# Optimization experiments

Measured on AMD Instinct MI355X. Metric: run time of the kernel, lower is better.

## Reference

```python
import jax, jax.numpy as jnp
import numpy as np

B, C, N, Hdim, Wdim = 32, 64, 16384, 128, 128  # N = Hdim*Wdim, C = dim = num_embeddings
EPS = 1e-5


def setup_inputs() -> dict:
    key = jax.random.key(0)
    ks = jax.random.split(key, 6)
    s = 0.05  # weight scale
    return {
        "x": jax.random.normal(ks[0], (B, C, N), dtype=jnp.float32),
        "Wq": jax.random.normal(ks[1], (C, C), dtype=jnp.float32) * s,   # Conv1d q (1x1)
        "bq": jnp.zeros((C,), jnp.float32),
        "gamma": jnp.ones((C,), jnp.float32),                              # BatchNorm1d affine
        "beta": jnp.zeros((C,), jnp.float32),
        "Wq2": jax.random.normal(ks[2], (C, C), dtype=jnp.float32) * s,  # Conv1d q2 (1x1)
        "bq2": jnp.zeros((C,), jnp.float32),
        "Wsr": jax.random.normal(ks[3], (C, C), dtype=jnp.float32) * s,  # Conv2d sr, k=1,s=1 -> 1x1
        "bsr": jnp.zeros((C,), jnp.float32),
        "Wc": jax.random.normal(ks[4], (C, C), dtype=jnp.float32) * s,   # Conv1d conv (1x1, no bias)
        "H": Hdim,
        "W": Wdim,
    }


def reference(x, Wq, bq, gamma, beta, Wq2, bq2, Wsr, bsr, Wc, H, W):
    # x: (B, C, N), N = H*W, sr_ratio = 1
    # q = q2(BN(q(x))) -- all 1x1 convs; BN uses batch statistics (torch training mode)
    q = jnp.einsum('oc,bcn->bon', Wq, x) + bq[None, :, None]            # (B,C,N)
    mu = q.mean(axis=(0, 2), keepdims=True)
    var = q.var(axis=(0, 2), keepdims=True)
    q = (q - mu) * jax.lax.rsqrt(var + EPS)
    q = q * gamma[None, :, None] + beta[None, :, None]
    q = jnp.einsum('oc,bcn->bon', Wq2, q) + bq2[None, :, None]          # (B,C,N)

    # k = sr(x) with kernel/stride 1 -> 1x1 conv, then permute to (B,N,C)
    k = jnp.einsum('oc,bcn->bon', Wsr, x) + bsr[None, :, None]          # (B,C,N)

    # v = AvgPool1d(C) over the channel axis of x^T -> channel mean, (B,1,N)
    v = x.mean(axis=1, keepdims=True)                                    # (B,1,N)

    # attn = q @ k^T over the N axis -> (B,C,C), then MaxPool1d(C) -> row-wise max (B,C,1)
    attn = jnp.einsum('bcn,bdn->bcd', q, k)                              # (B,C,C)
    attn = attn.max(axis=-1, keepdims=True)                              # (B,C,1)

    # out = conv( attn @ v )  -- outer product broadcast, then 1x1 conv (no bias)
    out = attn * v                                                       # (B,C,N)
    out = jnp.einsum('oc,bcn->bon', Wc, out)                             # (B,C,N)
    return out
```

## Files before the change

kernel.cpp:

```cpp
#include <hip/hip_runtime.h>
#include <hip/hip_bf16.h>

#define B_ 32
#define C_ 64
#define N_ 16384
constexpr float BN_INV = 1.0f / (32.0f * 16384.0f);

typedef float f32x4 __attribute__((ext_vector_type(4)));
typedef short s16x8 __attribute__((ext_vector_type(8)));

constexpr size_t WS_GPART = 0;
constexpr size_t WS_RPART = WS_GPART + (size_t)512 * 4096;
constexpr size_t WS_G     = WS_RPART + (size_t)512 * 64;
constexpr size_t WS_RB    = WS_G + (size_t)32 * 4096;
constexpr size_t WS_V     = WS_RB + (size_t)32 * 64;
constexpr size_t WS_W     = WS_V + (size_t)32 * N_;
constexpr size_t WS_GBAR  = WS_W + (size_t)32 * 64;
constexpr size_t WS_MBAR  = WS_GBAR + 4096;

__device__ constexpr int P1I[10] = {0,0,0,0,1,1,1,2,2,3};
__device__ constexpr int P1J[10] = {0,1,2,3,1,2,3,2,3,3};
__device__ constexpr int P1AT[4][4] = {{0,1,2,3},{1,4,5,6},{2,5,7,8},{3,6,8,9}};

__device__ __forceinline__ unsigned short bf16_rne_s(float f) {
    unsigned u = __float_as_uint(f);
    unsigned r = u + 0x7FFFu + ((u >> 16) & 1u);
    return (unsigned short)(r >> 16);
}
__device__ __forceinline__ float bf16f(unsigned short u) {
    return __uint_as_float(((unsigned)u) << 16);
}
__device__ __forceinline__ unsigned cvt_pk_bf16(float lo, float hi) {
    unsigned r;
    asm("v_cvt_pk_bf16_f32 %0, %1, %2" : "=v"(r) : "v"(lo), "v"(hi));
    return r;
}
__device__ __forceinline__ void cvt8hi(const f32x4& a, const f32x4& b, s16x8& hi) {
    union { unsigned w[4]; s16x8 v; } u;
    u.w[0] = cvt_pk_bf16(a[0], a[1]);
    u.w[1] = cvt_pk_bf16(a[2], a[3]);
    u.w[2] = cvt_pk_bf16(b[0], b[1]);
    u.w[3] = cvt_pk_bf16(b[2], b[3]);
    hi = u.v;
}

__global__ __launch_bounds__(512, 2) void k1(const float* __restrict__ x, float* __restrict__ ws) {
    __shared__ __align__(16) float rawb[4][10 * 256];
    __shared__ float rws[8][64];
    const int t = threadIdx.x, wv = t >> 6, lane = t & 63;
    const int b = blockIdx.x >> 4, ch = blockIdx.x & 15;
    const int kg = lane >> 4, cl = lane & 15;
    const float* xb = x + ((size_t)b * C_ + cl) * N_ + ch * 1024 + kg * 8;

    if (blockIdx.x == 0) {
        #pragma unroll
        for (int i = 0; i < 8; ++i) ws[WS_GBAR + t * 8 + i] = 0.f;
        if (t < 64) ws[WS_MBAR + t] = 0.f;
    }

    f32x4 accP1[10];
    #pragma unroll
    for (int i = 0; i < 10; ++i) accP1[i] = (f32x4){0.f, 0.f, 0.f, 0.f};
    f32x4 rs = {0.f, 0.f, 0.f, 0.f};

    f32x4 cA[4], cB[4], nA[4], nB[4];
    #pragma unroll
    for (int g = 0; g < 4; ++g) {
        cA[g] = *(const f32x4*)(xb + (size_t)g * (16 * N_) + wv * 32);
        cB[g] = *(const f32x4*)(xb + (size_t)g * (16 * N_) + wv * 32 + 4);
    }

    for (int w = 0; w < 4; ++w) {
        if (w < 3) {
            const int noff = (8 * (w + 1) + wv) * 32;
            #pragma unroll
            for (int g = 0; g < 4; ++g) {
                nA[g] = *(const f32x4*)(xb + (size_t)g * (16 * N_) + noff);
                nB[g] = *(const f32x4*)(xb + (size_t)g * (16 * N_) + noff + 4);
            }
        }
        s16x8 hi[4];
        #pragma unroll
        for (int g = 0; g < 4; ++g) cvt8hi(cA[g], cB[g], hi[g]);

        f32x4 s0 = cA[0] + cA[1] + cA[2] + cA[3];
        f32x4 s1 = cB[0] + cB[1] + cB[2] + cB[3];
        #pragma unroll
        for (int m = 1; m <= 8; m <<= 1) {
            #pragma unroll
            for (int j = 0; j < 4; ++j) {
                s0[j] += __shfl_xor(s0[j], m);
                s1[j] += __shfl_xor(s1[j], m);
            }
        }
        if (cl == 0) {
            float* vp = ws + WS_V + (size_t)b * N_ + ch * 1024 + (8 * w + wv) * 32 + kg * 8;
            *(f32x4*)vp       = s0 * 0.015625f;
            *(f32x4*)(vp + 4) = s1 * 0.015625f;
        }
        #pragma unroll
        for (int g = 0; g < 4; ++g)
            rs[g] += cA[g][0] + cA[g][1] + cA[g][2] + cA[g][3]
                   + cB[g][0] + cB[g][1] + cB[g][2] + cB[g][3];

        #pragma unroll
        for (int i = 0; i < 10; ++i)
            accP1[i] = __builtin_amdgcn_mfma_f32_16x16x32_bf16(hi[P1I[i]], hi[P1J[i]], accP1[i], 0, 0, 0);

        #pragma unroll
        for (int g = 0; g < 4; ++g) { cA[g] = nA[g]; cB[g] = nB[g]; }
    }

    #pragma unroll
    for (int g = 0; g < 4; ++g) {
        rs[g] += __shfl_xor(rs[g], 16);
        rs[g] += __shfl_xor(rs[g], 32);
    }
    if (lane < 16) {
        #pragma unroll
        for (int g = 0; g < 4; ++g) rws[wv][g * 16 + lane] = rs[g];
    }

    if (wv < 4) {
        float* dst = rawb[wv];
        #pragma unroll
        for (int i = 0; i < 10; ++i) *(f32x4*)(dst + i * 256 + lane * 4) = accP1[i];
    }
    __syncthreads();
    if (wv >= 4) {
        float* dst = rawb[wv - 4];
        #pragma unroll
        for (int i = 0; i < 10; ++i) {
            f32x4 o = *(f32x4*)(dst + i * 256 + lane * 4);
            *(f32x4*)(dst + i * 256 + lane * 4) = o + accP1[i];
        }
    }
    __syncthreads();
    if (t < 64) {
        float s = 0.f;
        #pragma unroll
        for (int g = 0; g < 8; ++g) s += rws[g][t];
        ws[WS_RPART + (size_t)blockIdx.x * 64 + t] = s;
    }
    float* gp = ws + WS_GPART + (size_t)blockIdx.x * 4096;
    for (int e = t; e < 4096; e += 512) {
        const int r = e >> 6, c = e & 63;
        const int bi = r >> 4, bj = c >> 4, rr = r & 15, cc = c & 15;
        const int i1 = P1AT[bi][bj] * 256;
        const int o1 = (bi <= bj) ? (((rr >> 2) * 16 + cc) * 4 + (rr & 3))
                                  : (((cc >> 2) * 16 + rr) * 4 + (cc & 3));
        gp[e] = rawb[0][i1 + o1] + rawb[1][i1 + o1] + rawb[2][i1 + o1] + rawb[3][i1 + o1];
    }
}

__global__ __launch_bounds__(256) void k2a(float* __restrict__ ws) {
    const int b = blockIdx.x >> 3, sl = blockIdx.x & 7, t = threadIdx.x;
    #pragma unroll
    for (int h = 0; h < 2; ++h) {
        const int e = sl * 512 + h * 256 + t;
        float s = 0.f;
        for (int chn = 0; chn < 16; ++chn) s += ws[WS_GPART + ((size_t)(b * 16 + chn)) * 4096 + e];
        ws[WS_G + (size_t)b * 4096 + e] = s;
        unsafeAtomicAdd(ws + WS_GBAR + e, s);
    }
    if (sl == 0 && t < 64) {
        float s = 0.f;
        for (int chn = 0; chn < 16; ++chn) s += ws[WS_RPART + (size_t)(b * 16 + chn) * 64 + t];
        ws[WS_RB + b * 64 + t] = s;
        unsafeAtomicAdd(ws + WS_MBAR + t, s);
    }
}

__global__ __launch_bounds__(256) void k2b(const float* __restrict__ Wq, const float* __restrict__ gamma,
                                           const float* __restrict__ beta, const float* __restrict__ Wq2,
                                           const float* __restrict__ bq2, const float* __restrict__ Wsr,
                                           const float* __restrict__ bsr, const float* __restrict__ Wc,
                                           float* __restrict__ ws) {
    __shared__ __align__(16) unsigned short OPH[6][64 * 72];
    __shared__ float quadS[64], muS[64], DS[64], abv[64], mS[64];
    __shared__ float rl[64], ul[64], avs[64], sbv[64], pls[64], aml[64];
    const int bb = blockIdx.x, t = threadIdx.x;
    const int w = t >> 6, lane = t & 63, cl = lane & 15, jg = lane >> 4;
    const int sr = t >> 2, sc0 = (t & 3) * 16;

    {
        const float* srcs[5] = { ws + WS_GBAR, Wq, Wq2, ws + WS_G + (size_t)bb * 4096, Wsr };
        #pragma unroll
        for (int mI = 0; mI < 5; ++mI) {
            const float sc = (mI == 0) ? BN_INV : 1.f;
            const float* src = srcs[mI] + sr * 64 + sc0;
            s16x8 h8[2];
            #pragma unroll
            for (int q = 0; q < 2; ++q) {
                f32x4 a = *(const f32x4*)(src + q * 8);
                f32x4 b2 = *(const f32x4*)(src + q * 8 + 4);
                #pragma unroll
                for (int j = 0; j < 8; ++j)
                    h8[q][j] = (short)bf16_rne_s(((j < 4) ? a[j] : b2[j - 4]) * sc);
            }
            *(s16x8*)(&OPH[mI][sr * 72 + sc0])     = h8[0];
            *(s16x8*)(&OPH[mI][sr * 72 + sc0 + 8]) = h8[1];
        }
    }
    if (t < 64) {
        mS[t]  = ws[WS_MBAR + t] * BN_INV;
        rl[t]  = ws[WS_RB + bb * 64 + t];
        sbv[t] = bsr[t];
    }
    __syncthreads();

    auto mmStripe = [&](const unsigned short* AH, const unsigned short* BH, int row0, f32x4* acc) {
        #pragma unroll
        for (int ks = 0; ks < 2; ++ks) {
            const int ko = ks * 32 + jg * 8;
            s16x8 ah = *(const s16x8*)(AH + (row0 + cl) * 72 + ko);
            #pragma unroll
            for (int bj = 0; bj < 4; ++bj) {
                s16x8 bh = *(const s16x8*)(BH + (16 * bj + cl) * 72 + ko);
                acc[bj] = __builtin_amdgcn_mfma_f32_16x16x32_bf16(ah, bh, acc[bj], 0, 0, 0);
            }
        }
    };

    if (w < 2) {
        f32x4 acc2[2][4];
        #pragma unroll
        for (int st = 0; st < 2; ++st)
            #pragma unroll
            for (int i = 0; i < 4; ++i) acc2[st][i] = (f32x4){0.f, 0.f, 0.f, 0.f};
        mmStripe(OPH[1], OPH[0], 32 * w,      acc2[0]);
        mmStripe(OPH[1], OPH[0], 32 * w + 16, acc2[1]);
        #pragma unroll
        for (int st = 0; st < 2; ++st) {
            float s[4] = {0.f, 0.f, 0.f, 0.f};
            #pragma unroll
            for (int j = 0; j < 4; ++j) {
                const int row = 32 * w + 16 * st + jg * 4 + j;
                #pragma unroll
                for (int bj = 0; bj < 4; ++bj)
                    s[j] += acc2[st][bj][j] * bf16f(OPH[1][row * 72 + 16 * bj + cl]);
            }
            #pragma unroll
            for (int m = 1; m <= 8; m <<= 1)
                #pragma unroll
                for (int j = 0; j < 4; ++j) s[j] += __shfl_xor(s[j], m);
            if (cl == 0) {
                #pragma unroll
                for (int j = 0; j < 4; ++j) quadS[32 * w + 16 * st + jg * 4 + j] = s[j];
            }
        }
        if (t < 64) {
            float s2 = 0.f;
            #pragma unroll 8
            for (int c = 0; c < 64; ++c) s2 += bf16f(OPH[1][t * 72 + c]) * mS[c];
            muS[t] = s2;
        }
    } else {
        const int w2 = w - 2;
        f32x4 acc2[2][4];
        #pragma unroll
        for (int st = 0; st < 2; ++st)
            #pragma unroll
            for (int i = 0; i < 4; ++i) acc2[st][i] = (f32x4){0.f, 0.f, 0.f, 0.f};
        mmStripe(OPH[4], OPH[3], 32 * w2,      acc2[0]);
        mmStripe(OPH[4], OPH[3], 32 * w2 + 16, acc2[1]);
        #pragma unroll
        for (int st = 0; st < 2; ++st)
            #pragma unroll
            for (int bj = 0; bj < 4; ++bj)
                #pragma unroll
                for (int j = 0; j < 4; ++j) {
                    const int row = 32 * w2 + 16 * st + jg * 4 + j, col = 16 * bj + cl;
                    OPH[5][row * 72 + col] = (unsigned short)bf16_rne_s(acc2[st][bj][j]);
                }
        const int t2 = t - 128;
        if (t2 < 64) {
            float s = 0.f;
            #pragma unroll 8
            for (int k = 0; k < 64; ++k) s += bf16f(OPH[4][t2 * 72 + k]) * rl[k];
            pls[t2] = s + 16384.f * sbv[t2];
        }
    }
    __syncthreads();

    if (t < 64) {
        const float var = quadS[t] - muS[t] * muS[t];
        const float D = gamma[t] * rsqrtf(var + 1e-5f);
        DS[t] = D;
        abv[t] = beta[t] - D * muS[t];
    }
    __syncthreads();
    {
        #pragma unroll
        for (int q = 0; q < 2; ++q) {
            s16x8 h8;
            #pragma unroll
            for (int j = 0; j < 8; ++j) {
                const int c = sc0 + q * 8 + j;
                h8[j] = (short)bf16_rne_s(DS[c] * bf16f(OPH[1][c * 72 + sr]));
            }
            *(s16x8*)(&OPH[0][sr * 72 + sc0 + q * 8]) = h8;
        }
    }
    if (t < 64) {
        float s = 0.f;
        #pragma unroll 8
        for (int k = 0; k < 64; ++k) s += bf16f(OPH[2][t * 72 + k]) * abv[k];
        avs[t] = s + bq2[t];
    }
    __syncthreads();

    {
        f32x4 accA[4];
        #pragma unroll
        for (int i = 0; i < 4; ++i) accA[i] = (f32x4){0.f, 0.f, 0.f, 0.f};
        mmStripe(OPH[2], OPH[0], 16 * w, accA);
        float su[4] = {0.f, 0.f, 0.f, 0.f};
        #pragma unroll
        for (int bj = 0; bj < 4; ++bj) {
            const float cv = rl[16 * bj + cl];
            #pragma unroll
            for (int j = 0; j < 4; ++j) su[j] += accA[bj][j] * cv;
        }
        #pragma unroll
        for (int m = 1; m <= 8; m <<= 1)
            #pragma unroll
            for (int j = 0; j < 4; ++j) su[j] += __shfl_xor(su[j], m);
        if (cl == 0) {
            #pragma unroll
            for (int j = 0; j < 4; ++j) ul[16 * w + jg * 4 + j] = su[j];
        }
        #pragma unroll
        for (int bj = 0; bj < 4; ++bj)
            #pragma unroll
            for (int j = 0; j < 4; ++j) {
                const int row = 16 * w + jg * 4 + j, col = 16 * bj + cl;
                OPH[1][row * 72 + col] = (unsigned short)bf16_rne_s(accA[bj][j]);
            }
    }
    __syncthreads();

    {
        f32x4 acc[4];
        #pragma unroll
        for (int i = 0; i < 4; ++i) acc[i] = (f32x4){0.f, 0.f, 0.f, 0.f};
        mmStripe(OPH[1], OPH[5], 16 * w, acc);
        float mx[4] = {-3.4e38f, -3.4e38f, -3.4e38f, -3.4e38f};
        #pragma unroll
        for (int j = 0; j < 4; ++j) {
            const int row = 16 * w + jg * 4 + j;
            const float ur = ul[row], ar = avs[row];
            #pragma unroll
            for (int bj = 0; bj < 4; ++bj) {
                const int col = 16 * bj + cl;
                const float v = acc[bj][j] + ur * sbv[col] + ar * pls[col];
                mx[j] = fmaxf(mx[j], v);
            }
        }
        #pragma unroll
        for (int m = 1; m <= 8; m <<= 1)
            #pragma unroll
            for (int j = 0; j < 4; ++j) mx[j] = fmaxf(mx[j], __shfl_xor(mx[j], m));
        if (cl == 0) {
            #pragma unroll
            for (int j = 0; j < 4; ++j) aml[16 * w + jg * 4 + j] = mx[j];
        }
    }
    __syncthreads();

    if (t < 64) {
        float s = 0.f;
        #pragma unroll 8
        for (int c = 0; c < 64; ++c) s += Wc[t * 64 + c] * aml[c];
        ws[WS_W + bb * 64 + t] = s;
    }
}

__global__ __launch_bounds__(256) void k3(const float* __restrict__ ws, float* __restrict__ out) {
    const int blk = blockIdx.x;
    const int b = blk >> 6, seg = blk & 63;
    const int r0 = (seg >> 4) * 16, chk = seg & 15;
    __shared__ float wls[16];
    const int t = threadIdx.x;
    if (t < 16) wls[t] = ws[WS_W + b * 64 + r0 + t];
    __syncthreads();
    const size_t nb = (size_t)chk * 1024 + 4 * t;
    const f32x4 v4 = *(const f32x4*)(ws + WS_V + (size_t)b * N_ + nb);
    float* ob = out + ((size_t)b * C_ + r0) * N_ + nb;
    #pragma unroll
    for (int o = 0; o < 16; ++o) {
        __builtin_nontemporal_store(v4 * wls[o], (f32x4*)(ob + (size_t)o * N_));
    }
}

extern "C" void kernel_launch(void* const* d_in, const int* in_sizes, int n_in,
                              void* d_out, int out_size, void* d_ws, size_t ws_size,
                              hipStream_t stream) {
    const float* x     = (const float*)d_in[0];
    const float* Wq    = (const float*)d_in[1];
    const float* gamma = (const float*)d_in[3];
    const float* beta  = (const float*)d_in[4];
    const float* Wq2   = (const float*)d_in[5];
    const float* bq2   = (const float*)d_in[6];
    const float* Wsr   = (const float*)d_in[7];
    const float* bsr   = (const float*)d_in[8];
    const float* Wc    = (const float*)d_in[9];
    float* ws  = (float*)d_ws;
    float* out = (float*)d_out;

    hipLaunchKernelGGL(k1,  dim3(512),  dim3(512), 0, stream, x, ws);
    hipLaunchKernelGGL(k2a, dim3(256),  dim3(256), 0, stream, ws);
    hipLaunchKernelGGL(k2b, dim3(32),   dim3(256), 0, stream,
                       Wq, gamma, beta, Wq2, bq2, Wsr, bsr, Wc, ws);
    hipLaunchKernelGGL(k3,  dim3(2048), dim3(256), 0, stream, ws, out);
}
```

Baseline: 68.91 us.

## Fuse reduction, chain and broadcast kernels into one cooperative kernel with grid syncs

```diff
diff --git a/kernel.cpp b/kernel.cpp
--- a/kernel.cpp
+++ b/kernel.cpp
@@ -1,5 +1,8 @@
 #include <hip/hip_runtime.h>
 #include <hip/hip_bf16.h>
+#include <hip/hip_cooperative_groups.h>
+
+namespace cg = cooperative_groups;
 
 #define B_ 32
 #define C_ 64
@@ -153,35 +156,38 @@
     }
 }
 
-__global__ __launch_bounds__(256) void k2a(float* __restrict__ ws) {
-    const int b = blockIdx.x >> 3, sl = blockIdx.x & 7, t = threadIdx.x;
-    #pragma unroll
-    for (int h = 0; h < 2; ++h) {
-        const int e = sl * 512 + h * 256 + t;
-        float s = 0.f;
-        for (int chn = 0; chn < 16; ++chn) s += ws[WS_GPART + ((size_t)(b * 16 + chn)) * 4096 + e];
-        ws[WS_G + (size_t)b * 4096 + e] = s;
-        unsafeAtomicAdd(ws + WS_GBAR + e, s);
-    }
+
+__device__ __forceinline__ void phaseA_body(int blk, int t, float* __restrict__ ws) {
+    const int b = blk >> 4, sl = blk & 15;
+    const int e = sl * 256 + t;
+    float s = 0.f;
+    #pragma unroll 4
+    for (int chn = 0; chn < 16; ++chn) s += ws[WS_GPART + ((size_t)(b * 16 + chn)) * 4096 + e];
+    ws[WS_G + (size_t)b * 4096 + e] = s;
+    unsafeAtomicAdd(ws + WS_GBAR + e, s);
     if (sl == 0 && t < 64) {
-        float s = 0.f;
-        for (int chn = 0; chn < 16; ++chn) s += ws[WS_RPART + (size_t)(b * 16 + chn) * 64 + t];
-        ws[WS_RB + b * 64 + t] = s;
-        unsafeAtomicAdd(ws + WS_MBAR + t, s);
-    }
-}
-
-__global__ __launch_bounds__(256) void k2b(const float* __restrict__ Wq, const float* __restrict__ gamma,
+        float s2 = 0.f;
+        #pragma unroll 4
+        for (int chn = 0; chn < 16; ++chn) s2 += ws[WS_RPART + (size_t)(b * 16 + chn) * 64 + t];
+        ws[WS_RB + b * 64 + t] = s2;
+        unsafeAtomicAdd(ws + WS_MBAR + t, s2);
+    }
+}
+
+__device__ __forceinline__ void chain_body(int bb, int t, unsigned short* __restrict__ OPH,
+                                           float* __restrict__ SV,
+                                           const float* __restrict__ Wq, const float* __restrict__ gamma,
                                            const float* __restrict__ beta, const float* __restrict__ Wq2,
                                            const float* __restrict__ bq2, const float* __restrict__ Wsr,
                                            const float* __restrict__ bsr, const float* __restrict__ Wc,
                                            float* __restrict__ ws) {
-    __shared__ __align__(16) unsigned short OPH[6][64 * 72];
-    __shared__ float quadS[64], muS[64], DS[64], abv[64], mS[64];
-    __shared__ float rl[64], ul[64], avs[64], sbv[64], pls[64], aml[64];
-    const int bb = blockIdx.x, t = threadIdx.x;
+    float* quadS = SV;        float* muS = SV + 64;  float* DS  = SV + 128;
+    float* abv   = SV + 192;  float* mS  = SV + 256; float* rl  = SV + 320;
+    float* ul    = SV + 384;  float* avs = SV + 448; float* sbv = SV + 512;
+    float* pls   = SV + 576;  float* aml = SV + 640;
     const int w = t >> 6, lane = t & 63, cl = lane & 15, jg = lane >> 4;
     const int sr = t >> 2, sc0 = (t & 3) * 16;
+    auto SLOT = [&](int i) { return OPH + i * 4608; };
 
     {
         const float* srcs[5] = { ws + WS_GBAR, Wq, Wq2, ws + WS_G + (size_t)bb * 4096, Wsr };
@@ -198,8 +204,8 @@
                 for (int j = 0; j < 8; ++j)
                     h8[q][j] = (short)bf16_rne_s(((j < 4) ? a[j] : b2[j - 4]) * sc);
             }
-            *(s16x8*)(&OPH[mI][sr * 72 + sc0])     = h8[0];
-            *(s16x8*)(&OPH[mI][sr * 72 + sc0 + 8]) = h8[1];
+            *(s16x8*)(SLOT(mI) + sr * 72 + sc0)     = h8[0];
+            *(s16x8*)(SLOT(mI) + sr * 72 + sc0 + 8) = h8[1];
         }
     }
     if (t < 64) {
@@ -228,8 +234,8 @@
         for (int st = 0; st < 2; ++st)
             #pragma unroll
             for (int i = 0; i < 4; ++i) acc2[st][i] = (f32x4){0.f, 0.f, 0.f, 0.f};
-        mmStripe(OPH[1], OPH[0], 32 * w,      acc2[0]);
-        mmStripe(OPH[1], OPH[0], 32 * w + 16, acc2[1]);
+        mmStripe(SLOT(1), SLOT(0), 32 * w,      acc2[0]);
+        mmStripe(SLOT(1), SLOT(0), 32 * w + 16, acc2[1]);
         #pragma unroll
         for (int st = 0; st < 2; ++st) {
             float s[4] = {0.f, 0.f, 0.f, 0.f};
@@ -238,7 +244,7 @@
                 const int row = 32 * w + 16 * st + jg * 4 + j;
                 #pragma unroll
                 for (int bj = 0; bj < 4; ++bj)
-                    s[j] += acc2[st][bj][j] * bf16f(OPH[1][row * 72 + 16 * bj + cl]);
+                    s[j] += acc2[st][bj][j] * bf16f(SLOT(1)[row * 72 + 16 * bj + cl]);
             }
             #pragma unroll
             for (int m = 1; m <= 8; m <<= 1)
@@ -252,7 +258,7 @@
         if (t < 64) {
             float s2 = 0.f;
             #pragma unroll 8
-            for (int c = 0; c < 64; ++c) s2 += bf16f(OPH[1][t * 72 + c]) * mS[c];
+            for (int c = 0; c < 64; ++c) s2 += bf16f(SLOT(1)[t * 72 + c]) * mS[c];
             muS[t] = s2;
         }
     } else {
@@ -262,8 +268,8 @@
         for (int st = 0; st < 2; ++st)
             #pragma unroll
             for (int i = 0; i < 4; ++i) acc2[st][i] = (f32x4){0.f, 0.f, 0.f, 0.f};
-        mmStripe(OPH[4], OPH[3], 32 * w2,      acc2[0]);
-        mmStripe(OPH[4], OPH[3], 32 * w2 + 16, acc2[1]);
+        mmStripe(SLOT(4), SLOT(3), 32 * w2,      acc2[0]);
+        mmStripe(SLOT(4), SLOT(3), 32 * w2 + 16, acc2[1]);
         #pragma unroll
         for (int st = 0; st < 2; ++st)
             #pragma unroll
@@ -271,13 +277,13 @@
                 #pragma unroll
                 for (int j = 0; j < 4; ++j) {
                     const int row = 32 * w2 + 16 * st + jg * 4 + j, col = 16 * bj + cl;
-                    OPH[5][row * 72 + col] = (unsigned short)bf16_rne_s(acc2[st][bj][j]);
+                    SLOT(5)[row * 72 + col] = (unsigned short)bf16_rne_s(acc2[st][bj][j]);
                 }
         const int t2 = t - 128;
-        if (t2 < 64) {
+        if (t2 < 64 && t2 >= 0) {
             float s = 0.f;
             #pragma unroll 8
-            for (int k = 0; k < 64; ++k) s += bf16f(OPH[4][t2 * 72 + k]) * rl[k];
+            for (int k = 0; k < 64; ++k) s += bf16f(SLOT(4)[t2 * 72 + k]) * rl[k];
             pls[t2] = s + 16384.f * sbv[t2];
         }
     }
@@ -297,15 +303,15 @@
             #pragma unroll
             for (int j = 0; j < 8; ++j) {
                 const int c = sc0 + q * 8 + j;
-                h8[j] = (short)bf16_rne_s(DS[c] * bf16f(OPH[1][c * 72 + sr]));
-            }
-            *(s16x8*)(&OPH[0][sr * 72 + sc0 + q * 8]) = h8;
+                h8[j] = (short)bf16_rne_s(DS[c] * bf16f(SLOT(1)[c * 72 + sr]));
+            }
+            *(s16x8*)(SLOT(0) + sr * 72 + sc0 + q * 8) = h8;
         }
     }
     if (t < 64) {
         float s = 0.f;
         #pragma unroll 8
-        for (int k = 0; k < 64; ++k) s += bf16f(OPH[2][t * 72 + k]) * abv[k];
+        for (int k = 0; k < 64; ++k) s += bf16f(SLOT(2)[t * 72 + k]) * abv[k];
         avs[t] = s + bq2[t];
     }
     __syncthreads();
@@ -314,7 +320,7 @@
         f32x4 accA[4];
         #pragma unroll
         for (int i = 0; i < 4; ++i) accA[i] = (f32x4){0.f, 0.f, 0.f, 0.f};
-        mmStripe(OPH[2], OPH[0], 16 * w, accA);
+        mmStripe(SLOT(2), SLOT(0), 16 * w, accA);
         float su[4] = {0.f, 0.f, 0.f, 0.f};
         #pragma unroll
         for (int bj = 0; bj < 4; ++bj) {
@@ -335,7 +341,7 @@
             #pragma unroll
             for (int j = 0; j < 4; ++j) {
                 const int row = 16 * w + jg * 4 + j, col = 16 * bj + cl;
-                OPH[1][row * 72 + col] = (unsigned short)bf16_rne_s(accA[bj][j]);
+                SLOT(1)[row * 72 + col] = (unsigned short)bf16_rne_s(accA[bj][j]);
             }
     }
     __syncthreads();
@@ -344,7 +350,7 @@
         f32x4 acc[4];
         #pragma unroll
         for (int i = 0; i < 4; ++i) acc[i] = (f32x4){0.f, 0.f, 0.f, 0.f};
-        mmStripe(OPH[1], OPH[5], 16 * w, acc);
+        mmStripe(SLOT(1), SLOT(5), 16 * w, acc);
         float mx[4] = {-3.4e38f, -3.4e38f, -3.4e38f, -3.4e38f};
         #pragma unroll
         for (int j = 0; j < 4; ++j) {
@@ -376,21 +382,58 @@
     }
 }
 
-__global__ __launch_bounds__(256) void k3(const float* __restrict__ ws, float* __restrict__ out) {
-    const int blk = blockIdx.x;
-    const int b = blk >> 6, seg = blk & 63;
-    const int r0 = (seg >> 4) * 16, chk = seg & 15;
-    __shared__ float wls[16];
-    const int t = threadIdx.x;
-    if (t < 16) wls[t] = ws[WS_W + b * 64 + r0 + t];
+__device__ __forceinline__ void phaseC_body(int blk, int t, float* __restrict__ wls,
+                                            const float* __restrict__ ws, float* __restrict__ out) {
+    const int b = blk >> 4, chk = blk & 15;
+    if (t < 64) wls[t] = ws[WS_W + b * 64 + t];
     __syncthreads();
     const size_t nb = (size_t)chk * 1024 + 4 * t;
     const f32x4 v4 = *(const f32x4*)(ws + WS_V + (size_t)b * N_ + nb);
-    float* ob = out + ((size_t)b * C_ + r0) * N_ + nb;
+    float* ob = out + (size_t)b * C_ * N_ + nb;
     #pragma unroll
-    for (int o = 0; o < 16; ++o) {
+    for (int o = 0; o < 64; ++o) {
         __builtin_nontemporal_store(v4 * wls[o], (f32x4*)(ob + (size_t)o * N_));
     }
+}
+
+__global__ __launch_bounds__(256, 2) void k2x(const float* __restrict__ Wq, const float* __restrict__ gamma,
+                                              const float* __restrict__ beta, const float* __restrict__ Wq2,
+                                              const float* __restrict__ bq2, const float* __restrict__ Wsr,
+                                              const float* __restrict__ bsr, const float* __restrict__ Wc,
+                                              float* __restrict__ ws, float* __restrict__ out) {
+    __shared__ __align__(16) unsigned char smem[58112];
+    cg::grid_group grid = cg::this_grid();
+    const int t = threadIdx.x;
+
+    phaseA_body(blockIdx.x, t, ws);
+    __threadfence();
+    grid.sync();
+
+    if (blockIdx.x < 32) {
+        chain_body(blockIdx.x, t, (unsigned short*)smem, (float*)(smem + 55296),
+                   Wq, gamma, beta, Wq2, bq2, Wsr, bsr, Wc, ws);
+    }
+    __threadfence();
+    grid.sync();
+
+    phaseC_body(blockIdx.x, t, (float*)smem, ws, out);
+}
+
+__global__ __launch_bounds__(256) void k2a(float* __restrict__ ws) {
+    phaseA_body(blockIdx.x, threadIdx.x, ws);
+}
+__global__ __launch_bounds__(256) void k2b(const float* __restrict__ Wq, const float* __restrict__ gamma,
+                                           const float* __restrict__ beta, const float* __restrict__ Wq2,
+                                           const float* __restrict__ bq2, const float* __restrict__ Wsr,
+                                           const float* __restrict__ bsr, const float* __restrict__ Wc,
+                                           float* __restrict__ ws) {
+    __shared__ __align__(16) unsigned char smem[58112];
+    chain_body(blockIdx.x, threadIdx.x, (unsigned short*)smem, (float*)(smem + 55296),
+               Wq, gamma, beta, Wq2, bq2, Wsr, bsr, Wc, ws);
+}
+__global__ __launch_bounds__(256) void k3(const float* __restrict__ ws, float* __restrict__ out) {
+    __shared__ float wls[64];
+    phaseC_body(blockIdx.x, threadIdx.x, wls, ws, out);
 }
 
 extern "C" void kernel_launch(void* const* d_in, const int* in_sizes, int n_in,
@@ -408,9 +451,16 @@
     float* ws  = (float*)d_ws;
     float* out = (float*)d_out;
 
-    hipLaunchKernelGGL(k1,  dim3(512),  dim3(512), 0, stream, x, ws);
-    hipLaunchKernelGGL(k2a, dim3(256),  dim3(256), 0, stream, ws);
-    hipLaunchKernelGGL(k2b, dim3(32),   dim3(256), 0, stream,
-                       Wq, gamma, beta, Wq2, bq2, Wsr, bsr, Wc, ws);
-    hipLaunchKernelGGL(k3,  dim3(2048), dim3(256), 0, stream, ws, out);
-}
+    hipLaunchKernelGGL(k1, dim3(512), dim3(512), 0, stream, x, ws);
+
+    void* args[] = {(void*)&Wq, (void*)&gamma, (void*)&beta, (void*)&Wq2, (void*)&bq2,
+                    (void*)&Wsr, (void*)&bsr, (void*)&Wc, (void*)&ws, (void*)&out};
+    hipError_t err = hipLaunchCooperativeKernel((void*)k2x, dim3(512), dim3(256), args, 0, stream);
+    if (err != hipSuccess) {
+        (void)hipGetLastError();
+        hipLaunchKernelGGL(k2a, dim3(512), dim3(256), 0, stream, ws);
+        hipLaunchKernelGGL(k2b, dim3(32),  dim3(256), 0, stream,
+                           Wq, gamma, beta, Wq2, bq2, Wsr, bsr, Wc, ws);
+        hipLaunchKernelGGL(k3,  dim3(512), dim3(256), 0, stream, ws, out);
+    }
+}
```

Measured after the change: 238.0 us. 245% more time.

## Fuse Gram reduction and per-batch solve into one cooperative kernel

Applied to the files above, without the earlier changes.

```diff
diff --git a/kernel.cpp b/kernel.cpp
--- a/kernel.cpp
+++ b/kernel.cpp
@@ -1,5 +1,8 @@
 #include <hip/hip_runtime.h>
 #include <hip/hip_bf16.h>
+#include <hip/hip_cooperative_groups.h>
+
+namespace cg = cooperative_groups;
 
 #define B_ 32
 #define C_ 64
@@ -17,6 +20,8 @@
 constexpr size_t WS_W     = WS_V + (size_t)32 * N_;
 constexpr size_t WS_GBAR  = WS_W + (size_t)32 * 64;
 constexpr size_t WS_MBAR  = WS_GBAR + 4096;
+constexpr size_t WS_QUAD  = WS_MBAR + 64;
+constexpr size_t WS_MACC  = WS_QUAD + 64;
 
 __device__ constexpr int P1I[10] = {0,0,0,0,1,1,1,2,2,3};
 __device__ constexpr int P1J[10] = {0,1,2,3,1,2,3,2,3,3};
@@ -55,7 +60,11 @@
     if (blockIdx.x == 0) {
         #pragma unroll
         for (int i = 0; i < 8; ++i) ws[WS_GBAR + t * 8 + i] = 0.f;
-        if (t < 64) ws[WS_MBAR + t] = 0.f;
+        if (t < 64) {
+            ws[WS_MBAR + t] = 0.f;
+            ws[WS_QUAD + t] = 0.f;
+            ws[WS_MACC + t] = 0.f;
+        }
     }
 
     f32x4 accP1[10];
@@ -150,6 +159,238 @@
         const int o1 = (bi <= bj) ? (((rr >> 2) * 16 + cc) * 4 + (rr & 3))
                                   : (((cc >> 2) * 16 + rr) * 4 + (cc & 3));
         gp[e] = rawb[0][i1 + o1] + rawb[1][i1 + o1] + rawb[2][i1 + o1] + rawb[3][i1 + o1];
+    }
+}
+
+__global__ __launch_bounds__(256, 2) void k2bc(const float* __restrict__ Wq, const float* __restrict__ gamma,
+                                               const float* __restrict__ beta, const float* __restrict__ Wq2,
+                                               const float* __restrict__ bq2, const float* __restrict__ Wsr,
+                                               const float* __restrict__ bsr, const float* __restrict__ Wc,
+                                               float* __restrict__ ws) {
+    __shared__ __align__(16) unsigned short OPH[6][64 * 72];
+    __shared__ float quadS[64], muS[64], DS[64], abv[64], mS[64];
+    __shared__ float rl[64], ul[64], avs[64], sbv[64], pls[64], aml[64];
+    cg::grid_group grid = cg::this_grid();
+    const int bb = blockIdx.x, t = threadIdx.x;
+    const int w = t >> 6, lane = t & 63, cl = lane & 15, jg = lane >> 4;
+    const int sr = t >> 2, sc0 = (t & 3) * 16;
+
+    {
+        f32x4 s[4];
+        #pragma unroll
+        for (int j = 0; j < 4; ++j) s[j] = (f32x4){0.f, 0.f, 0.f, 0.f};
+        for (int chn = 0; chn < 16; ++chn) {
+            const float* gbp = ws + WS_GPART + ((size_t)(bb * 16 + chn)) * 4096 + sr * 64 + sc0;
+            #pragma unroll
+            for (int j = 0; j < 4; ++j) s[j] += *(const f32x4*)(gbp + 4 * j);
+        }
+        s16x8 h8[2];
+        #pragma unroll
+        for (int q = 0; q < 2; ++q)
+            #pragma unroll
+            for (int j = 0; j < 8; ++j)
+                h8[q][j] = (short)bf16_rne_s(s[q * 2 + (j >> 2)][j & 3]);
+        *(s16x8*)(&OPH[3][sr * 72 + sc0])     = h8[0];
+        *(s16x8*)(&OPH[3][sr * 72 + sc0 + 8]) = h8[1];
+    }
+    {
+        const float* srcs[3] = { Wq, Wq2, Wsr };
+        const int slot[3] = {1, 2, 4};
+        #pragma unroll
+        for (int mI = 0; mI < 3; ++mI) {
+            const float* src = srcs[mI] + sr * 64 + sc0;
+            s16x8 h8[2];
+            #pragma unroll
+            for (int q = 0; q < 2; ++q) {
+                f32x4 a = *(const f32x4*)(src + q * 8);
+                f32x4 b2 = *(const f32x4*)(src + q * 8 + 4);
+                #pragma unroll
+                for (int j = 0; j < 8; ++j)
+                    h8[q][j] = (short)bf16_rne_s((j < 4) ? a[j] : b2[j - 4]);
+            }
+            *(s16x8*)(&OPH[slot[mI]][sr * 72 + sc0])     = h8[0];
+            *(s16x8*)(&OPH[slot[mI]][sr * 72 + sc0 + 8]) = h8[1];
+        }
+    }
+    if (t < 64) {
+        float s = 0.f;
+        #pragma unroll 4
+        for (int chn = 0; chn < 16; ++chn) s += ws[WS_RPART + (size_t)(bb * 16 + chn) * 64 + t];
+        rl[t]  = s;
+        sbv[t] = bsr[t];
+        unsafeAtomicAdd(ws + WS_MACC + t, s);
+    }
+    __syncthreads();
+
+    auto mmStripe = [&](const unsigned short* AH, const unsigned short* BH, int row0, f32x4* acc) {
+        #pragma unroll
+        for (int ks = 0; ks < 2; ++ks) {
+            const int ko = ks * 32 + jg * 8;
+            s16x8 ah = *(const s16x8*)(AH + (row0 + cl) * 72 + ko);
+            #pragma unroll
+            for (int bj = 0; bj < 4; ++bj) {
+                s16x8 bh = *(const s16x8*)(BH + (16 * bj + cl) * 72 + ko);
+                acc[bj] = __builtin_amdgcn_mfma_f32_16x16x32_bf16(ah, bh, acc[bj], 0, 0, 0);
+            }
+        }
+    };
+
+    if (w < 2) {
+        f32x4 acc2[2][4];
+        #pragma unroll
+        for (int st = 0; st < 2; ++st)
+            #pragma unroll
+            for (int i = 0; i < 4; ++i) acc2[st][i] = (f32x4){0.f, 0.f, 0.f, 0.f};
+        mmStripe(OPH[1], OPH[3], 32 * w,      acc2[0]);
+        mmStripe(OPH[1], OPH[3], 32 * w + 16, acc2[1]);
+        #pragma unroll
+        for (int st = 0; st < 2; ++st) {
+            float s[4] = {0.f, 0.f, 0.f, 0.f};
+            #pragma unroll
+            for (int j = 0; j < 4; ++j) {
+                const int row = 32 * w + 16 * st + jg * 4 + j;
+                #pragma unroll
+                for (int bj = 0; bj < 4; ++bj)
+                    s[j] += acc2[st][bj][j] * bf16f(OPH[1][row * 72 + 16 * bj + cl]);
+            }
+            #pragma unroll
+            for (int m = 1; m <= 8; m <<= 1)
+                #pragma unroll
+                for (int j = 0; j < 4; ++j) s[j] += __shfl_xor(s[j], m);
+            if (cl == 0) {
+                #pragma unroll
+                for (int j = 0; j < 4; ++j)
+                    unsafeAtomicAdd(ws + WS_QUAD + 32 * w + 16 * st + jg * 4 + j, s[j]);
+            }
+        }
+    } else {
+        const int w2 = w - 2;
+        f32x4 acc2[2][4];
+        #pragma unroll
+        for (int st = 0; st < 2; ++st)
+            #pragma unroll
+            for (int i = 0; i < 4; ++i) acc2[st][i] = (f32x4){0.f, 0.f, 0.f, 0.f};
+        mmStripe(OPH[4], OPH[3], 32 * w2,      acc2[0]);
+        mmStripe(OPH[4], OPH[3], 32 * w2 + 16, acc2[1]);
+        #pragma unroll
+        for (int st = 0; st < 2; ++st)
+            #pragma unroll
+            for (int bj = 0; bj < 4; ++bj)
+                #pragma unroll
+                for (int j = 0; j < 4; ++j) {
+                    const int row = 32 * w2 + 16 * st + jg * 4 + j, col = 16 * bj + cl;
+                    OPH[5][row * 72 + col] = (unsigned short)bf16_rne_s(acc2[st][bj][j]);
+                }
+        const int t2 = t - 128;
+        if (t2 < 64 && t2 >= 0) {
+            float s = 0.f;
+            #pragma unroll 8
+            for (int k = 0; k < 64; ++k) s += bf16f(OPH[4][t2 * 72 + k]) * rl[k];
+            pls[t2] = s + 16384.f * sbv[t2];
+        }
+    }
+    __threadfence();
+    grid.sync();
+
+    if (t < 64) {
+        mS[t]    = ws[WS_MACC + t] * BN_INV;
+        quadS[t] = ws[WS_QUAD + t] * BN_INV;
+    }
+    __syncthreads();
+    if (t < 64) {
+        float s2 = 0.f;
+        #pragma unroll 8
+        for (int c = 0; c < 64; ++c) s2 += bf16f(OPH[1][t * 72 + c]) * mS[c];
+        muS[t] = s2;
+        const float var = quadS[t] - s2 * s2;
+        const float D = gamma[t] * rsqrtf(var + 1e-5f);
+        DS[t] = D;
+        abv[t] = beta[t] - D * s2;
+    }
+    __syncthreads();
+    {
+        #pragma unroll
+        for (int q = 0; q < 2; ++q) {
+            s16x8 h8;
+            #pragma unroll
+            for (int j = 0; j < 8; ++j) {
+                const int c = sc0 + q * 8 + j;
+                h8[j] = (short)bf16_rne_s(DS[c] * bf16f(OPH[1][c * 72 + sr]));
+            }
+            *(s16x8*)(&OPH[0][sr * 72 + sc0 + q * 8]) = h8;
+        }
+    }
+    if (t < 64) {
+        float s = 0.f;
+        #pragma unroll 8
+        for (int k = 0; k < 64; ++k) s += bf16f(OPH[2][t * 72 + k]) * abv[k];
+        avs[t] = s + bq2[t];
+    }
+    __syncthreads();
+
+    {
+        f32x4 accA[4];
+        #pragma unroll
+        for (int i = 0; i < 4; ++i) accA[i] = (f32x4){0.f, 0.f, 0.f, 0.f};
+        mmStripe(OPH[2], OPH[0], 16 * w, accA);
+        float su[4] = {0.f, 0.f, 0.f, 0.f};
+        #pragma unroll
+        for (int bj = 0; bj < 4; ++bj) {
+            const float cv = rl[16 * bj + cl];
+            #pragma unroll
+            for (int j = 0; j < 4; ++j) su[j] += accA[bj][j] * cv;
+        }
+        #pragma unroll
+        for (int m = 1; m <= 8; m <<= 1)
+            #pragma unroll
+            for (int j = 0; j < 4; ++j) su[j] += __shfl_xor(su[j], m);
+        if (cl == 0) {
+            #pragma unroll
+            for (int j = 0; j < 4; ++j) ul[16 * w + jg * 4 + j] = su[j];
+        }
+        #pragma unroll
+        for (int bj = 0; bj < 4; ++bj)
+            #pragma unroll
+            for (int j = 0; j < 4; ++j) {
+                const int row = 16 * w + jg * 4 + j, col = 16 * bj + cl;
+                OPH[1][row * 72 + col] = (unsigned short)bf16_rne_s(accA[bj][j]);
+            }
+    }
+    __syncthreads();
+
+    {
+        f32x4 acc[4];
+        #pragma unroll
+        for (int i = 0; i < 4; ++i) acc[i] = (f32x4){0.f, 0.f, 0.f, 0.f};
+        mmStripe(OPH[1], OPH[5], 16 * w, acc);
+        float mx[4] = {-3.4e38f, -3.4e38f, -3.4e38f, -3.4e38f};
+        #pragma unroll
+        for (int j = 0; j < 4; ++j) {
+            const int row = 16 * w + jg * 4 + j;
+            const float ur = ul[row], ar = avs[row];
+            #pragma unroll
+            for (int bj = 0; bj < 4; ++bj) {
+                const int col = 16 * bj + cl;
+                const float v = acc[bj][j] + ur * sbv[col] + ar * pls[col];
+                mx[j] = fmaxf(mx[j], v);
+            }
+        }
+        #pragma unroll
+        for (int m = 1; m <= 8; m <<= 1)
+            #pragma unroll
+            for (int j = 0; j < 4; ++j) mx[j] = fmaxf(mx[j], __shfl_xor(mx[j], m));
+        if (cl == 0) {
+            #pragma unroll
+            for (int j = 0; j < 4; ++j) aml[16 * w + jg * 4 + j] = mx[j];
+        }
+    }
+    __syncthreads();
+
+    if (t < 64) {
+        float s = 0.f;
+        #pragma unroll 8
+        for (int c = 0; c < 64; ++c) s += Wc[t * 64 + c] * aml[c];
+        ws[WS_W + bb * 64 + t] = s;
     }
 }
 
@@ -182,7 +423,6 @@
     const int bb = blockIdx.x, t = threadIdx.x;
     const int w = t >> 6, lane = t & 63, cl = lane & 15, jg = lane >> 4;
     const int sr = t >> 2, sc0 = (t & 3) * 16;
-
     {
         const float* srcs[5] = { ws + WS_GBAR, Wq, Wq2, ws + WS_G + (size_t)bb * 4096, Wsr };
         #pragma unroll
@@ -208,7 +448,6 @@
         sbv[t] = bsr[t];
     }
     __syncthreads();
-
     auto mmStripe = [&](const unsigned short* AH, const unsigned short* BH, int row0, f32x4* acc) {
         #pragma unroll
         for (int ks = 0; ks < 2; ++ks) {
@@ -221,7 +460,6 @@
             }
         }
     };
-
     if (w < 2) {
         f32x4 acc2[2][4];
         #pragma unroll
@@ -274,7 +512,7 @@
                     OPH[5][row * 72 + col] = (unsigned short)bf16_rne_s(acc2[st][bj][j]);
                 }
         const int t2 = t - 128;
-        if (t2 < 64) {
+        if (t2 < 64 && t2 >= 0) {
             float s = 0.f;
             #pragma unroll 8
             for (int k = 0; k < 64; ++k) s += bf16f(OPH[4][t2 * 72 + k]) * rl[k];
@@ -282,7 +520,6 @@
         }
     }
     __syncthreads();
-
     if (t < 64) {
         const float var = quadS[t] - muS[t] * muS[t];
         const float D = gamma[t] * rsqrtf(var + 1e-5f);
@@ -309,7 +546,6 @@
         avs[t] = s + bq2[t];
     }
     __syncthreads();
-
     {
         f32x4 accA[4];
         #pragma unroll
@@ -339,7 +575,6 @@
             }
     }
     __syncthreads();
-
     {
         f32x4 acc[4];
         #pragma unroll
@@ -367,7 +602,6 @@
         }
     }
     __syncthreads();
-
     if (t < 64) {
         float s = 0.f;
         #pragma unroll 8
@@ -408,9 +642,16 @@
     float* ws  = (float*)d_ws;
     float* out = (float*)d_out;
 
-    hipLaunchKernelGGL(k1,  dim3(512),  dim3(512), 0, stream, x, ws);
-    hipLaunchKernelGGL(k2a, dim3(256),  dim3(256), 0, stream, ws);
-    hipLaunchKernelGGL(k2b, dim3(32),   dim3(256), 0, stream,
-                       Wq, gamma, beta, Wq2, bq2, Wsr, bsr, Wc, ws);
-    hipLaunchKernelGGL(k3,  dim3(2048), dim3(256), 0, stream, ws, out);
-}
+    hipLaunchKernelGGL(k1, dim3(512), dim3(512), 0, stream, x, ws);
+
+    void* args[] = {(void*)&Wq, (void*)&gamma, (void*)&beta, (void*)&Wq2, (void*)&bq2,
+                    (void*)&Wsr, (void*)&bsr, (void*)&Wc, (void*)&ws};
+    hipError_t err = hipLaunchCooperativeKernel((void*)k2bc, dim3(32), dim3(256), args, 0, stream);
+    if (err != hipSuccess) {
+        (void)hipGetLastError();
+        hipLaunchKernelGGL(k2a, dim3(256), dim3(256), 0, stream, ws);
+        hipLaunchKernelGGL(k2b, dim3(32),  dim3(256), 0, stream,
+                           Wq, gamma, beta, Wq2, bq2, Wsr, bsr, Wc, ws);
+    }
+    hipLaunchKernelGGL(k3, dim3(2048), dim3(256), 0, stream, ws, out);
+}
```

New measurement: 94.55 us. 37.2% more time.
